# Optimization experiments

Hardware: AMD Instinct MI355X
Metric: run time of the kernel (lower is better)

Reference implementation:

```python
import jax, jax.numpy as jnp
import numpy as np

N_HEADS = 16

def _rotate_half(x):
    half = x.shape[-1] // 2
    x1, x2 = x[..., :half], x[..., half:]
    return jnp.concatenate([-x2, x1], axis=-1)

def setup_inputs() -> dict:
    key = jax.random.key(0)
    ks = jax.random.split(key, 6)
    B, L, D = 8, 1024, 1280
    hd = D // N_HEADS
    return {
        "hidden_states": jax.random.normal(ks[0], (B, L, D), dtype=jnp.float32),
        "rotary_pos_emb": jax.random.normal(ks[1], (L, hd // 2), dtype=jnp.float32),
        "W_qkv": jax.random.normal(ks[2], (D, 3 * D), dtype=jnp.float32) * 0.02,
        "b_qkv": jax.random.normal(ks[3], (3 * D,), dtype=jnp.float32) * 0.02,
        "W_proj": jax.random.normal(ks[4], (D, D), dtype=jnp.float32) * 0.02,
        "b_proj": jax.random.normal(ks[5], (D,), dtype=jnp.float32) * 0.02,
    }

def reference(hidden_states, rotary_pos_emb, W_qkv, b_qkv, W_proj, b_proj):
    B, L, D = hidden_states.shape
    H = N_HEADS
    hd = D // H
    # QKV projection -> [3, B, H, L, hd]
    qkv = (hidden_states @ W_qkv + b_qkv).reshape(B, L, 3, H, hd)
    qkv = jnp.transpose(qkv, (2, 0, 3, 1, 4))
    q, k, v = qkv[0], qkv[1], qkv[2]
    # rotary embedding: emb = cat([freqs, freqs]) -> [L, hd], broadcast [1,1,L,hd]
    emb = jnp.concatenate([rotary_pos_emb, rotary_pos_emb], axis=-1)
    cos = jnp.cos(emb)[None, None]
    sin = jnp.sin(emb)[None, None]
    q = q * cos + _rotate_half(q) * sin
    k = k * cos + _rotate_half(k) * sin
    # causal SDPA (cu_seqlens is None => is_causal=True)
    scale = 1.0 / jnp.sqrt(jnp.asarray(hd, dtype=q.dtype))
    scores = jnp.einsum("bhqd,bhkd->bhqk", q, k) * scale
    causal = jnp.tril(jnp.ones((L, L), dtype=bool))
    scores = jnp.where(causal, scores, jnp.finfo(scores.dtype).min)
    attn = jax.nn.softmax(scores, axis=-1)
    out = jnp.einsum("bhqk,bhkd->bhqd", attn, v)  # [B,H,L,hd]
    out = jnp.transpose(out, (0, 2, 1, 3)).reshape(B, L, D)
    return out @ W_proj + b_proj
```

## Files before the change

kernel.cpp:

```cpp
#include <hip/hip_runtime.h>
#include <hip/hip_bf16.h>
#include <stdint.h>

#define DEV static __device__ __forceinline__

typedef __attribute__((ext_vector_type(4))) float  f32x4;
typedef __attribute__((ext_vector_type(8))) __bf16 bf16x8;
typedef __attribute__((ext_vector_type(8))) unsigned short u16x8;
typedef __attribute__((ext_vector_type(4))) unsigned short u16x4;
typedef __attribute__((ext_vector_type(4))) float  fvec4;

#define SC2F 0.16129870963914802f

DEV unsigned short f2b(float f) {
  __bf16 h = (__bf16)f;
  unsigned short u; __builtin_memcpy(&u, &h, 2);
  return u;
}
DEV float b2f(unsigned short b) {
  union { unsigned int u; float f; } v; v.u = ((unsigned int)b) << 16;
  return v.f;
}
DEV bf16x8 bzero8() {
  u16x8 z = 0; bf16x8 r; __builtin_memcpy(&r, &z, 16); return r;
}

DEV void gload_lds16(const void* g, void* l) {
  __builtin_amdgcn_global_load_lds(
      (__attribute__((address_space(1))) void*)(uintptr_t)g,
      (__attribute__((address_space(3))) void*)(uintptr_t)l, 16, 0, 0);
}


__global__ void convert_bf16x4(const float* __restrict__ in,
                               unsigned short* __restrict__ out, int n4) {
  int i = blockIdx.x * 256 + threadIdx.x;
  if (i >= n4) return;
  fvec4 v = *(const fvec4*)&in[(size_t)i * 4];
  u16x4 o;
  o[0] = f2b(v[0]); o[1] = f2b(v[1]); o[2] = f2b(v[2]); o[3] = f2b(v[3]);
  *(u16x4*)&out[(size_t)i * 4] = o;
}

__global__ void transpose_f2b(const float* __restrict__ in,
                              unsigned short* __restrict__ out, int R, int C) {
  __shared__ float t[32][33];
  int c0 = blockIdx.x * 32, r0 = blockIdx.y * 32;
  int tx = threadIdx.x & 31, ty = threadIdx.x >> 5;
#pragma unroll
  for (int i = 0; i < 32; i += 8)
    t[ty + i][tx] = in[(size_t)(r0 + ty + i) * C + c0 + tx];
  __syncthreads();
#pragma unroll
  for (int i = 0; i < 32; i += 8)
    out[(size_t)(c0 + ty + i) * R + r0 + tx] = f2b(t[tx][ty + i]);
}

__global__ void rope_table(const float* __restrict__ r, float* __restrict__ c,
                           float* __restrict__ s, int n) {
  int i = blockIdx.x * 256 + threadIdx.x;
  if (i < n) { float v = r[i]; c[i] = cosf(v); s[i] = sinf(v); }
}

template <int EPI>
__global__ __launch_bounds__(256) void gemm128(
    const unsigned short* __restrict__ A, const unsigned short* __restrict__ Bt,
    const float* __restrict__ bias,
    unsigned short* __restrict__ qo, unsigned short* __restrict__ ko,
    unsigned short* __restrict__ vo, float* __restrict__ outf,
    int M, int N, int K) {
  __shared__ __align__(16) unsigned short As[128 * 64];
  __shared__ __align__(16) unsigned short Bs[128 * 64];
  const int tid = threadIdx.x;
  const int lane = tid & 63, wave = tid >> 6;
  const int wr = wave >> 1, wc = wave & 1;
  const int g = lane >> 4, lr = lane & 15;
  const int nwg = gridDim.x, cpx = nwg >> 3;
  const int swz = (blockIdx.x & 7) * cpx + (blockIdx.x >> 3);
  const int gx = N >> 7;
  const int bx = swz % gx, by = swz / gx;
  const int m0 = by * 128, n0 = bx * 128;

  f32x4 acc[4][4];
#pragma unroll
  for (int i = 0; i < 4; ++i)
#pragma unroll
    for (int j = 0; j < 4; ++j) acc[i][j] = f32x4{0.f, 0.f, 0.f, 0.f};

  for (int k0 = 0; k0 < K; k0 += 64) {
#pragma unroll
    for (int it = 0; it < 4; ++it) {
      int e = (it * 256 + tid) * 8;
      int r = e >> 6, p = (e >> 3) & 7;
      int sc = ((p ^ (r & 7)) << 3);
      gload_lds16(&A[(size_t)(m0 + r) * K + k0 + sc], &As[e]);
      gload_lds16(&Bt[(size_t)(n0 + r) * K + k0 + sc], &Bs[e]);
    }
    __syncthreads();
#pragma unroll
    for (int kk = 0; kk < 2; ++kk) {
      bf16x8 av[4], bv[4];
#pragma unroll
      for (int mf = 0; mf < 4; ++mf) {
        int row = wr * 64 + mf * 16 + lr;
        int ch = (kk * 4 + g) ^ (row & 7);
        av[mf] = *(const bf16x8*)&As[row * 64 + ch * 8];
      }
#pragma unroll
      for (int nf = 0; nf < 4; ++nf) {
        int row = wc * 64 + nf * 16 + lr;
        int ch = (kk * 4 + g) ^ (row & 7);
        bv[nf] = *(const bf16x8*)&Bs[row * 64 + ch * 8];
      }
#pragma unroll
      for (int mf = 0; mf < 4; ++mf)
#pragma unroll
        for (int nf = 0; nf < 4; ++nf)
          acc[mf][nf] = __builtin_amdgcn_mfma_f32_16x16x32_bf16(
              av[mf], bv[nf], acc[mf][nf], 0, 0, 0);
    }
    __syncthreads();
  }

  if (EPI == 0) {
#pragma unroll
    for (int nf = 0; nf < 4; ++nf) {
      int col = n0 + wc * 64 + nf * 16 + lr;
      float bvv = bias[col];
      int s = col / 1280;
      int rem = col - s * 1280;
      int h = rem / 80, d = rem - h * 80;
      unsigned short* dst = (s == 0) ? qo : ((s == 1) ? ko : vo);
#pragma unroll
      for (int mf = 0; mf < 4; ++mf) {
#pragma unroll
        for (int r = 0; r < 4; ++r) {
          int row = m0 + wr * 64 + mf * 16 + g * 4 + r;
          int b = row >> 10, l = row & 1023;
          dst[((size_t)(b * 16 + h) * 1024 + l) * 80 + d] =
              f2b(acc[mf][nf][r] + bvv);
        }
      }
    }
  } else {
#pragma unroll
    for (int mf = 0; mf < 4; ++mf) {
#pragma unroll
      for (int r = 0; r < 4; ++r) {
        int row = m0 + wr * 64 + mf * 16 + g * 4 + r;
#pragma unroll
        for (int nf = 0; nf < 4; ++nf) {
          int col = n0 + wc * 64 + nf * 16 + lr;
          outf[(size_t)row * N + col] = acc[mf][nf][r] + bias[col];
        }
      }
    }
  }
}

__global__ void rope_apply(unsigned short* __restrict__ q0,
                           unsigned short* __restrict__ q1,
                           const float* __restrict__ cosT,
                           const float* __restrict__ sinT) {
  int i = blockIdx.x * 256 + threadIdx.x;
  if (i >= 2 * 131072 * 5) return;
  bool isq = (i < 131072 * 5);
  unsigned short* arr = isq ? q0 : q1;
  float sc = isq ? SC2F : 1.0f;
  int rem = isq ? i : (i - 131072 * 5);
  int row = rem / 5, c = rem - (rem / 5) * 5;
  int l = row & 1023;
  size_t base = (size_t)row * 80 + c * 8;
  u16x8 x1 = *(const u16x8*)&arr[base];
  u16x8 x2 = *(const u16x8*)&arr[base + 40];
  const float* cp = &cosT[l * 40 + c * 8];
  const float* sp = &sinT[l * 40 + c * 8];
  u16x8 y1, y2;
#pragma unroll
  for (int j = 0; j < 8; ++j) {
    float a = b2f(x1[j]), b = b2f(x2[j]);
    float cc = cp[j], ss = sp[j];
    y1[j] = f2b((a * cc - b * ss) * sc);
    y2[j] = f2b((b * cc + a * ss) * sc);
  }
  *(u16x8*)&arr[base] = y1;
  *(u16x8*)&arr[base + 40] = y2;
}

__global__ __launch_bounds__(512, 4) void attn_fwd(
    const unsigned short* __restrict__ q, const unsigned short* __restrict__ k,
    const unsigned short* __restrict__ v, unsigned short* __restrict__ o) {
  __shared__ __align__(16) unsigned short Ks[2][5120];
  __shared__ __align__(16) unsigned short Vt[2][5760];
  __shared__ __align__(16) unsigned short Ps[8][2304];

  const int tid = threadIdx.x, lane = tid & 63, wave = tid >> 6;
  const int g = lane >> 4, lr = lane & 15;
  const int bid = blockIdx.x;
  const int t4 = bid >> 7;
  const int qi = (t4 == 0) ? 3 : (t4 == 1) ? 2 : (t4 == 2) ? 0 : 1;
  const int bh = bid & 127;
  const int b = bh >> 4, h = bh & 15;
  const size_t headBase = (size_t)bh * 1024 * 80;
  const int qbase = qi * 256;
  const int wmin = qbase + wave * 32;
  const int nkv = qi * 4 + 4;
  const int vl = tid & 63, vc = tid >> 6;

  bf16x8 qf[2][2], qf2[2];
#pragma unroll
  for (int mf = 0; mf < 2; ++mf) {
    const unsigned short* qr = q + headBase + (size_t)(wmin + mf * 16 + lr) * 80;
    qf[mf][0] = *(const bf16x8*)(qr + g * 8);
    qf[mf][1] = *(const bf16x8*)(qr + 32 + g * 8);
    bf16x8 t = *(const bf16x8*)(qr + 64 + (g & 1) * 8);
    if (g >= 2) t = bzero8();
    qf2[mf] = t;
  }

  float m_r[2] = {-INFINITY, -INFINITY}, l_r[2] = {0.f, 0.f};
  f32x4 o_acc[2][5];
#pragma unroll
  for (int mf = 0; mf < 2; ++mf)
#pragma unroll
    for (int of = 0; of < 5; ++of) o_acc[mf][of] = f32x4{0.f, 0.f, 0.f, 0.f};

  unsigned short* PsW = Ps[wave];

  {
    const unsigned short* vsrc = v + headBase;
    u16x8 p0 = *(const u16x8*)&vsrc[(size_t)vl * 80 + vc * 8];
    u16x8 p1;
    if (tid < 128) p1 = *(const u16x8*)&vsrc[(size_t)vl * 80 + (8 + vc) * 8];
    for (int i = tid; i < 640; i += 512)
      gload_lds16(k + headBase + i * 8, &Ks[0][i * 8]);
#pragma unroll
    for (int j = 0; j < 8; ++j) Vt[0][(vc * 8 + j) * 72 + vl] = p0[j];
    if (tid < 128) {
#pragma unroll
      for (int j = 0; j < 8; ++j) Vt[0][((8 + vc) * 8 + j) * 72 + vl] = p1[j];
    }
  }
  __syncthreads();

  for (int kv = 0; kv < nkv; ++kv) {
    const int bufI = kv & 1, nb = bufI ^ 1;
    const int kvbase = kv * 64;
    const bool doStage = (kv + 1 < nkv);
    const bool active = (kvbase <= wmin + 31);

    u16x8 p0, p1;
    if (doStage) {
      const unsigned short* vsrc = v + headBase + (size_t)(kv + 1) * 5120;
      p0 = *(const u16x8*)&vsrc[(size_t)vl * 80 + vc * 8];
      if (tid < 128) p1 = *(const u16x8*)&vsrc[(size_t)vl * 80 + (8 + vc) * 8];
      const unsigned short* ksrc = k + headBase + (size_t)(kv + 1) * 5120;
      for (int i = tid; i < 640; i += 512)
        gload_lds16(ksrc + i * 8, &Ks[nb][i * 8]);
    }

    if (active) {
      const unsigned short* KsB = Ks[bufI];
      f32x4 s[2][4];
#pragma unroll
      for (int mf = 0; mf < 2; ++mf)
#pragma unroll
        for (int nf = 0; nf < 4; ++nf) s[mf][nf] = f32x4{0.f, 0.f, 0.f, 0.f};
#pragma unroll
      for (int kp = 0; kp < 2; ++kp)
#pragma unroll
        for (int nf = 0; nf < 4; ++nf) {
          bf16x8 kb = *(const bf16x8*)&KsB[(nf * 16 + lr) * 80 + kp * 32 + g * 8];
#pragma unroll
          for (int mf = 0; mf < 2; ++mf)
            s[mf][nf] = __builtin_amdgcn_mfma_f32_16x16x32_bf16(kb, qf[mf][kp],
                                                                s[mf][nf], 0, 0, 0);
        }
#pragma unroll
      for (int nf = 0; nf < 4; ++nf) {
        bf16x8 kb = *(const bf16x8*)&KsB[(nf * 16 + lr) * 80 + 64 + (g & 1) * 8];
#pragma unroll
        for (int mf = 0; mf < 2; ++mf)
          s[mf][nf] = __builtin_amdgcn_mfma_f32_16x16x32_bf16(kb, qf2[mf],
                                                              s[mf][nf], 0, 0, 0);
      }

      const bool maskT = (kvbase + 63 > wmin);
      if (maskT) {
        const int kb0 = kvbase + g * 4;
        const int qq = wmin + lr;
#pragma unroll
        for (int mf = 0; mf < 2; ++mf)
#pragma unroll
          for (int nf = 0; nf < 4; ++nf)
#pragma unroll
            for (int r = 0; r < 4; ++r)
              if (kb0 + nf * 16 + r > qq + mf * 16) s[mf][nf][r] = -INFINITY;
      }
      float mt[2];
#pragma unroll
      for (int mf = 0; mf < 2; ++mf) {
        float a = fmaxf(fmaxf(s[mf][0][0], s[mf][0][1]), fmaxf(s[mf][0][2], s[mf][0][3]));
        float b2 = fmaxf(fmaxf(s[mf][1][0], s[mf][1][1]), fmaxf(s[mf][1][2], s[mf][1][3]));
        float c = fmaxf(fmaxf(s[mf][2][0], s[mf][2][1]), fmaxf(s[mf][2][2], s[mf][2][3]));
        float d = fmaxf(fmaxf(s[mf][3][0], s[mf][3][1]), fmaxf(s[mf][3][2], s[mf][3][3]));
        float m = fmaxf(fmaxf(a, b2), fmaxf(c, d));
        m = fmaxf(m, __shfl_xor(m, 16, 64));
        m = fmaxf(m, __shfl_xor(m, 32, 64));
        mt[mf] = m;
      }
      int ok = (mt[0] <= m_r[0] + 10.0f) && (mt[1] <= m_r[1] + 10.0f);
      const bool need = !__all(ok);
      float fr[2];
      if (need) {
#pragma unroll
        for (int mf = 0; mf < 2; ++mf) {
          float mn = fmaxf(m_r[mf], mt[mf]);
          fr[mf] = exp2f(m_r[mf] - mn);
          m_r[mf] = mn;
        }
      }
      float lt[2] = {0.f, 0.f};
#pragma unroll
      for (int mf = 0; mf < 2; ++mf)
#pragma unroll
        for (int nf = 0; nf < 4; ++nf)
#pragma unroll
          for (int r = 0; r < 4; ++r) {
            float p = exp2f(s[mf][nf][r] - m_r[mf]);
            s[mf][nf][r] = p;
            lt[mf] += p;
          }
#pragma unroll
      for (int mf = 0; mf < 2; ++mf) {
        lt[mf] += __shfl_xor(lt[mf], 16, 64);
        lt[mf] += __shfl_xor(lt[mf], 32, 64);
      }
      if (need) {
#pragma unroll
        for (int mf = 0; mf < 2; ++mf) {
          l_r[mf] = l_r[mf] * fr[mf] + lt[mf];
#pragma unroll
          for (int r = 0; r < 4; ++r) {
            float fro = __shfl(fr[mf], g * 4 + r, 64);
#pragma unroll
            for (int of = 0; of < 5; ++of) o_acc[mf][of][r] *= fro;
          }
        }
      } else {
        l_r[0] += lt[0];
        l_r[1] += lt[1];
      }

#pragma unroll
      for (int mf = 0; mf < 2; ++mf)
#pragma unroll
        for (int nf = 0; nf < 4; ++nf) {
          unsigned w0 = (unsigned)f2b(s[mf][nf][0]) |
                        ((unsigned)f2b(s[mf][nf][1]) << 16);
          unsigned w1 = (unsigned)f2b(s[mf][nf][2]) |
                        ((unsigned)f2b(s[mf][nf][3]) << 16);
          unsigned* dst = (unsigned*)&PsW[(mf * 16 + lr) * 72 + nf * 16 + g * 4];
          dst[0] = w0;
          dst[1] = w1;
        }
    }

    if (doStage) {
#pragma unroll
      for (int j = 0; j < 8; ++j) Vt[nb][(vc * 8 + j) * 72 + vl] = p0[j];
      if (tid < 128) {
#pragma unroll
        for (int j = 0; j < 8; ++j) Vt[nb][((8 + vc) * 8 + j) * 72 + vl] = p1[j];
      }
    }

    if (active) {
      const unsigned short* VtB = Vt[bufI];
#pragma unroll
      for (int kk = 0; kk < 2; ++kk) {
        bf16x8 pa[2];
#pragma unroll
        for (int mf = 0; mf < 2; ++mf)
          pa[mf] = *(const bf16x8*)&PsW[(mf * 16 + lr) * 72 + kk * 32 + g * 8];
#pragma unroll
        for (int of = 0; of < 5; ++of) {
          bf16x8 vv = *(const bf16x8*)&VtB[(of * 16 + lr) * 72 + kk * 32 + g * 8];
#pragma unroll
          for (int mf = 0; mf < 2; ++mf)
            o_acc[mf][of] = __builtin_amdgcn_mfma_f32_16x16x32_bf16(
                pa[mf], vv, o_acc[mf][of], 0, 0, 0);
        }
      }
    }
    __syncthreads();
  }

#pragma unroll
  for (int mf = 0; mf < 2; ++mf) {
    float linv = 1.0f / l_r[mf];
#pragma unroll
    for (int r = 0; r < 4; ++r) {
      float li = __shfl(linv, g * 4 + r, 64);
      int row = wmin + mf * 16 + g * 4 + r;
#pragma unroll
      for (int of = 0; of < 5; ++of)
        o[((size_t)b * 1024 + row) * 1280 + h * 80 + of * 16 + lr] =
            f2b(o_acc[mf][of][r] * li);
    }
  }
}

extern "C" void kernel_launch(void* const* d_in, const int* in_sizes, int n_in,
                              void* d_out, int out_size, void* d_ws, size_t ws_size,
                              hipStream_t stream) {
  const float* X     = (const float*)d_in[0];
  const float* rp    = (const float*)d_in[1];
  const float* Wqkv  = (const float*)d_in[2];
  const float* bqkv  = (const float*)d_in[3];
  const float* Wproj = (const float*)d_in[4];
  const float* bproj = (const float*)d_in[5];
  float* out = (float*)d_out;

  char* ws = (char*)d_ws;
  unsigned short* Xb     = (unsigned short*)(ws);
  unsigned short* Wqkvt  = (unsigned short*)(ws + 20971520);
  unsigned short* Wprojt = (unsigned short*)(ws + 30801920);
  float*          cosT   = (float*)(ws + 34078720);
  float*          sinT   = (float*)(ws + 34242560);
  unsigned short* vb     = (unsigned short*)(ws + 34406400);
  unsigned short* qb     = (unsigned short*)d_out;
  unsigned short* kb     = qb + 10485760;
  unsigned short* Ob     = Xb;

  convert_bf16x4<<<10240, 256, 0, stream>>>(X, Xb, 2621440);
  transpose_f2b<<<dim3(120, 40), 256, 0, stream>>>(Wqkv, Wqkvt, 1280, 3840);
  transpose_f2b<<<dim3(40, 40), 256, 0, stream>>>(Wproj, Wprojt, 1280, 1280);
  rope_table<<<160, 256, 0, stream>>>(rp, cosT, sinT, 40960);
  gemm128<0><<<1920, 256, 0, stream>>>(Xb, Wqkvt, bqkv, qb, kb, vb,
                                       nullptr, 8192, 3840, 1280);
  rope_apply<<<5120, 256, 0, stream>>>(qb, kb, cosT, sinT);
  attn_fwd<<<512, 512, 0, stream>>>(qb, kb, vb, Ob);
  gemm128<1><<<640, 256, 0, stream>>>(Ob, Wprojt, bproj, nullptr,
                                      nullptr, nullptr, out, 8192, 1280, 1280);
}
```

Before: 373.3 us.

## Use 256x256 double-buffered tile GEMM for QKV projection

Adds a gemm256 kernel with 256x256 output tiles, 8 waves per block and double-buffered LDS staging, and uses it for the QKV projection in place of the 128x128 gemm128. Larger tiles raise arithmetic intensity and halve global reloads of A and B, and the prefetch of the next K slice overlaps loads with MFMA. In exchange it uses 128 KB of LDS and many accumulator registers per block, which limits occupancy. The grid shrinks to 480 blocks, which may leave wave quantization imbalance across CUs.

```diff
diff --git a/kernel.cpp b/kernel.cpp
--- a/kernel.cpp
+++ b/kernel.cpp
@@ -60,6 +60,113 @@
                            float* __restrict__ s, int n) {
   int i = blockIdx.x * 256 + threadIdx.x;
   if (i < n) { float v = r[i]; c[i] = cosf(v); s[i] = sinf(v); }
+}
+
+template <int EPI>
+__global__ __launch_bounds__(512, 2) void gemm256(
+    const unsigned short* __restrict__ A, const unsigned short* __restrict__ Bt,
+    const float* __restrict__ bias,
+    unsigned short* __restrict__ qo, unsigned short* __restrict__ ko,
+    unsigned short* __restrict__ vo, float* __restrict__ outf,
+    int M, int N, int K) {
+  __shared__ __align__(16) unsigned short As[2][256 * 64];
+  __shared__ __align__(16) unsigned short Bs[2][256 * 64];
+  const int tid = threadIdx.x;
+  const int lane = tid & 63, wave = tid >> 6;
+  const int wr = wave >> 2, wc = wave & 3;
+  const int g = lane >> 4, lr = lane & 15;
+  const int nwg = gridDim.x, cpx = nwg >> 3;
+  const int swz = (blockIdx.x & 7) * cpx + (blockIdx.x >> 3);
+  const int gx = N >> 8;
+  const int bx = swz % gx, by = swz / gx;
+  const int m0 = by * 256, n0 = bx * 256;
+  const int nt = K >> 6;
+
+  f32x4 acc[8][4];
+#pragma unroll
+  for (int i = 0; i < 8; ++i)
+#pragma unroll
+    for (int j = 0; j < 4; ++j) acc[i][j] = f32x4{0.f, 0.f, 0.f, 0.f};
+
+#define STAGE256(bi, t)                                                       \
+  {                                                                           \
+    const int k0s = (t) * 64;                                                 \
+    _Pragma("unroll")                                                         \
+    for (int it = 0; it < 4; ++it) {                                          \
+      int e = (it * 512 + tid) * 8;                                           \
+      int r = e >> 6, p = (e >> 3) & 7;                                       \
+      int sc = ((p ^ (r & 7)) << 3);                                          \
+      gload_lds16(&A[(size_t)(m0 + r) * K + k0s + sc], &As[bi][e]);           \
+      gload_lds16(&Bt[(size_t)(n0 + r) * K + k0s + sc], &Bs[bi][e]);          \
+    }                                                                         \
+  }
+
+  STAGE256(0, 0);
+  __syncthreads();
+
+  for (int t = 0; t < nt; ++t) {
+    const int cur = t & 1;
+    if (t + 1 < nt) STAGE256(cur ^ 1, t + 1);
+#pragma unroll
+    for (int kk = 0; kk < 2; ++kk) {
+      bf16x8 av[8], bv[4];
+#pragma unroll
+      for (int mf = 0; mf < 8; ++mf) {
+        int row = wr * 128 + mf * 16 + lr;
+        int ch = (kk * 4 + g) ^ (row & 7);
+        av[mf] = *(const bf16x8*)&As[cur][row * 64 + ch * 8];
+      }
+#pragma unroll
+      for (int nf = 0; nf < 4; ++nf) {
+        int row = wc * 64 + nf * 16 + lr;
+        int ch = (kk * 4 + g) ^ (row & 7);
+        bv[nf] = *(const bf16x8*)&Bs[cur][row * 64 + ch * 8];
+      }
+#pragma unroll
+      for (int mf = 0; mf < 8; ++mf)
+#pragma unroll
+        for (int nf = 0; nf < 4; ++nf)
+          acc[mf][nf] = __builtin_amdgcn_mfma_f32_16x16x32_bf16(
+              av[mf], bv[nf], acc[mf][nf], 0, 0, 0);
+    }
+    __syncthreads();
+  }
+#undef STAGE256
+
+  if (EPI == 0) {
+#pragma unroll
+    for (int nf = 0; nf < 4; ++nf) {
+      int col = n0 + wc * 64 + nf * 16 + lr;
+      float bvv = bias[col];
+      int s = col / 1280;
+      int rem = col - s * 1280;
+      int h = rem / 80, d = rem - h * 80;
+      unsigned short* dst = (s == 0) ? qo : ((s == 1) ? ko : vo);
+#pragma unroll
+      for (int mf = 0; mf < 8; ++mf) {
+#pragma unroll
+        for (int r = 0; r < 4; ++r) {
+          int row = m0 + wr * 128 + mf * 16 + g * 4 + r;
+          int b = row >> 10, l = row & 1023;
+          dst[((size_t)(b * 16 + h) * 1024 + l) * 80 + d] =
+              f2b(acc[mf][nf][r] + bvv);
+        }
+      }
+    }
+  } else {
+#pragma unroll
+    for (int mf = 0; mf < 8; ++mf) {
+#pragma unroll
+      for (int r = 0; r < 4; ++r) {
+        int row = m0 + wr * 128 + mf * 16 + g * 4 + r;
+#pragma unroll
+        for (int nf = 0; nf < 4; ++nf) {
+          int col = n0 + wc * 64 + nf * 16 + lr;
+          outf[(size_t)row * N + col] = acc[mf][nf][r] + bias[col];
+        }
+      }
+    }
+  }
 }
 
 template <int EPI>
@@ -437,8 +544,8 @@
   transpose_f2b<<<dim3(120, 40), 256, 0, stream>>>(Wqkv, Wqkvt, 1280, 3840);
   transpose_f2b<<<dim3(40, 40), 256, 0, stream>>>(Wproj, Wprojt, 1280, 1280);
   rope_table<<<160, 256, 0, stream>>>(rp, cosT, sinT, 40960);
-  gemm128<0><<<1920, 256, 0, stream>>>(Xb, Wqkvt, bqkv, qb, kb, vb,
-                                       nullptr, 8192, 3840, 1280);
+  gemm256<0><<<480, 512, 0, stream>>>(Xb, Wqkvt, bqkv, qb, kb, vb,
+                                      nullptr, 8192, 3840, 1280);
   rope_apply<<<5120, 256, 0, stream>>>(qb, kb, cosT, sinT);
   attn_fwd<<<512, 512, 0, stream>>>(qb, kb, vb, Ob);
   gemm128<1><<<640, 256, 0, stream>>>(Ob, Wprojt, bproj, nullptr,
```

Result: faster. 349.2 us (-6.5%).
